# Kernel tuning notes

Hardware: AMD Instinct MI355X
Metric: run time of the kernel (lower is better)

Reference implementation:

```python
import jax, jax.numpy as jnp
import numpy as np

D_MODEL = 2048
N_HEADS = 8
EXPAND_K = 1
EXPAND_V = 2
DK = D_MODEL * EXPAND_K // N_HEADS      # 256 per-head key dim
DV = D_MODEL * EXPAND_V // N_HEADS      # 512 per-head value dim
INTER = 5632
EPS = 1e-6
CHUNK = 64


def setup_inputs() -> dict:
    key = jax.random.key(0)
    ks = jax.random.split(key, 12)
    d = D_MODEL
    s = lambda fan_in: 1.0 / np.sqrt(fan_in)
    return {
        "hidden_states": jax.random.normal(ks[0], (2, 2048, d), jnp.float32),
        "attn_norm_w": jnp.ones((d,), jnp.float32),
        "q_w": jax.random.normal(ks[1], (d, d * EXPAND_K), jnp.float32) * s(d),
        "k_w": jax.random.normal(ks[2], (d, d * EXPAND_K), jnp.float32) * s(d),
        "v_w": jax.random.normal(ks[3], (d, d * EXPAND_V), jnp.float32) * s(d),
        "g_w": jax.random.normal(ks[4], (d, d * EXPAND_V), jnp.float32) * s(d),
        "o_w": jax.random.normal(ks[5], (d * EXPAND_V, d), jnp.float32) * s(d * EXPAND_V),
        "gnorm_w": jnp.ones((DV,), jnp.float32),
        "mlp_norm_w": jnp.ones((d,), jnp.float32),
        "gate_w": jax.random.normal(ks[6], (d, INTER * 2), jnp.float32) * s(d),
        "down_w": jax.random.normal(ks[7], (INTER, d), jnp.float32) * s(INTER),
    }


def rmsnorm(x, w, eps=EPS):
    return x * jax.lax.rsqrt(jnp.mean(x * x, axis=-1, keepdims=True) + eps) * w


def rope(x):
    # x: [B, T, H, D]; non-interleaved rotary on full head dim
    T, D = x.shape[1], x.shape[-1]
    inv_freq = 1.0 / (10000.0 ** (jnp.arange(0, D, 2, dtype=jnp.float32) / D))
    ang = jnp.arange(T, dtype=jnp.float32)[:, None] * inv_freq  # [T, D/2]
    cos = jnp.cos(ang)[None, :, None, :]
    sin = jnp.sin(ang)[None, :, None, :]
    x1, x2 = jnp.split(x, 2, axis=-1)
    return jnp.concatenate([x1 * cos - x2 * sin, x2 * cos + x1 * sin], axis=-1)


def chunk_retention(q, k, v):
    # q,k: [B,T,H,Dk], v: [B,T,H,Dv]; chunkwise-recurrent RetNet retention
    B, T, H, Dk = q.shape
    Dv = v.shape[-1]
    C = CHUNK
    N = T // C
    gamma = 1.0 - jnp.exp2(-5.0 - jnp.arange(H, dtype=jnp.float32))  # [H]
    i = jnp.arange(C, dtype=jnp.float32)
    diff = i[:, None] - i[None, :]
    Dmask = jnp.where(diff >= 0, gamma[:, None, None] ** diff, 0.0)   # [H,C,C]
    cross_decay = gamma[:, None] ** (i[None, :] + 1.0)                # [H,C]
    k_decay = gamma[:, None] ** (C - 1.0 - i[None, :])                # [H,C]
    chunk_decay = gamma ** C                                          # [H]

    # -> [N, B, H, C, D]
    to_chunks = lambda x: jnp.moveaxis(
        x.reshape(B, N, C, H, x.shape[-1]).transpose(0, 1, 3, 2, 4), 1, 0)
    qc, kc, vc = to_chunks(q), to_chunks(k), to_chunks(v)

    def body(S, inp):
        qb, kb, vb = inp  # [B,H,C,Dk/Dv]
        attn = jnp.einsum('bhid,bhjd->bhij', qb, kb) * Dmask
        o_intra = jnp.einsum('bhij,bhje->bhie', attn, vb)
        o_cross = jnp.einsum('bhid,bhde->bhie', qb * cross_decay[None, :, :, None], S)
        S = chunk_decay[None, :, None, None] * S + \
            jnp.einsum('bhid,bhie->bhde', kb * k_decay[None, :, :, None], vb)
        return S, o_intra + o_cross

    S0 = jnp.zeros((B, H, Dk, Dv), q.dtype)
    _, o = jax.lax.scan(body, S0, (qc, kc, vc))  # o: [N,B,H,C,Dv]
    return jnp.moveaxis(o, 0, 1).transpose(0, 1, 3, 2, 4).reshape(B, T, H, Dv)


def reference(hidden_states, attn_norm_w, q_w, k_w, v_w, g_w, o_w, gnorm_w,
              mlp_norm_w, gate_w, down_w):
    B, T, d = hidden_states.shape
    residual = hidden_states
    h = rmsnorm(hidden_states, attn_norm_w)

    # MultiScaleRetention
    q = (h @ q_w).reshape(B, T, N_HEADS, DK)
    k = (h @ k_w).reshape(B, T, N_HEADS, DK)
    v = (h @ v_w).reshape(B, T, N_HEADS, DV)
    g = (h @ g_w).reshape(B, T, N_HEADS, DV)
    q, k = rope(q), rope(k)
    q = q * (DK ** -0.5)
    o = chunk_retention(q, k, v)
    # fused RMSNorm + swish gate (per head over Dv)
    o = rmsnorm(o, gnorm_w) * (g * jax.nn.sigmoid(g))
    h = o.reshape(B, T, N_HEADS * DV) @ o_w

    # fused-residual RMSNorm
    residual = h + residual
    h = rmsnorm(residual, mlp_norm_w)

    # SwiGLU MLP
    y = h @ gate_w
    gate, y = jnp.split(y, 2, axis=-1)
    h = (gate * jax.nn.sigmoid(gate) * y) @ down_w
    return residual + h
```

## Files before the change

kernel.cpp:

```cpp
#include <hip/hip_runtime.h>
#include <cstdint>
#include <cstddef>

typedef unsigned short u16;
typedef __attribute__((ext_vector_type(4))) float f32x4;
typedef __attribute__((ext_vector_type(4))) unsigned int u32x4;

__device__ __forceinline__ float b2f(u16 u) {
  union { unsigned int i; float f; } x; x.i = ((unsigned int)u) << 16; return x.f;
}
__device__ __forceinline__ u16 f2b(float f) {
  union { float f; unsigned int i; } x; x.f = f;
  unsigned int i = x.i;
  i += 0x7fffu + ((i >> 16) & 1u);
  return (u16)(i >> 16);
}

__device__ __forceinline__ void mfma_bf16(f32x4& c, u32x4 a, u32x4 b) {
  asm("v_mfma_f32_16x16x32_bf16 %0, %1, %2, %0" : "+v"(c) : "v"(a), "v"(b));
}

__device__ __forceinline__ void async_ld16(const u16* g, u16* l) {
  typedef __attribute__((address_space(1))) const unsigned int GU;
  typedef __attribute__((address_space(3))) unsigned int LU;
  __builtin_amdgcn_global_load_lds((GU*)g, (LU*)l, 16, 0, 0);
}

__global__ __launch_bounds__(256)
void transpose_cast_kernel(const float* __restrict__ in, u16* __restrict__ out,
                           int K, int N, int ldin) {
  __shared__ float tile[64][65];
  const int nb = N >> 6;
  const int bk = blockIdx.x / nb, bn = blockIdx.x % nb;
  const int k0 = bk * 64, n0 = bn * 64;
  const int tid = threadIdx.x;
#pragma unroll
  for (int p = 0; p < 16; ++p) {
    int idx = p * 256 + tid;
    int r = idx >> 6, c = idx & 63;
    tile[r][c] = in[(size_t)(k0 + r) * ldin + n0 + c];
  }
  __syncthreads();
#pragma unroll
  for (int p = 0; p < 16; ++p) {
    int idx = p * 256 + tid;
    int r = idx >> 6, c = idx & 63;
    out[(size_t)(n0 + r) * K + k0 + c] = f2b(tile[c][r]);
  }
}

__global__ __launch_bounds__(256)
void transpose_k_kernel(const u16* __restrict__ kb, u16* __restrict__ kt) {
  __shared__ u16 tile[64][72];
  const int bid = blockIdx.x;
  const int dd = bid & 3, tt = (bid >> 2) & 31;
  const int h = (bid >> 7) & 7, b = bid >> 10;
  const int t0 = tt * 64, d0 = dd * 64;
  const int tid = threadIdx.x;
#pragma unroll
  for (int p = 0; p < 2; ++p) {
    int idx = p * 256 + tid;
    int r = idx >> 3, cq = (idx & 7) * 8;
    *(uint4*)&tile[r][cq] =
        *(const uint4*)&kb[(size_t)(b * 2048 + t0 + r) * 2048 + h * 256 + d0 + cq];
  }
  __syncthreads();
#pragma unroll
  for (int p = 0; p < 2; ++p) {
    int idx = p * 256 + tid;
    int r = idx >> 3, cq = (idx & 7) * 8;
    union { u16 h8[8]; uint4 v4; } o;
#pragma unroll
    for (int j = 0; j < 8; ++j) o.h8[j] = tile[cq + j][r];
    *(uint4*)&kt[((size_t)(b * 8 + h) * 256 + d0 + r) * 2048 + t0 + cq] = o.v4;
  }
}

__global__ __launch_bounds__(256)
void rmsnorm_cast_kernel(const float* __restrict__ x, const float* __restrict__ w,
                         u16* __restrict__ out) {
  const int row = blockIdx.x, tid = threadIdx.x;
  const float* xr = x + (size_t)row * 2048;
  float4 a = ((const float4*)xr)[tid * 2];
  float4 b = ((const float4*)xr)[tid * 2 + 1];
  float ss = a.x*a.x + a.y*a.y + a.z*a.z + a.w*a.w
           + b.x*b.x + b.y*b.y + b.z*b.z + b.w*b.w;
#pragma unroll
  for (int m = 32; m; m >>= 1) ss += __shfl_xor(ss, m);
  __shared__ float ps[4];
  if ((tid & 63) == 0) ps[tid >> 6] = ss;
  __syncthreads();
  const float sc = rsqrtf((ps[0] + ps[1] + ps[2] + ps[3]) * (1.0f / 2048.0f) + 1e-6f);
  const int base = tid * 8;
  const float vals[8] = {a.x, a.y, a.z, a.w, b.x, b.y, b.z, b.w};
  union { u16 h[8]; uint4 v4[2]; } o;
#pragma unroll
  for (int j = 0; j < 8; ++j) o.h[j] = f2b(vals[j] * sc * w[base + j]);
  *(uint4*)&out[(size_t)row * 2048 + base] = o.v4[0];
  *(uint4*)&out[(size_t)row * 2048 + base + 8] = o.v4[1];
}

__global__ __launch_bounds__(256)
void rmsnorm_bf16_kernel(const u16* __restrict__ x, const float* __restrict__ w,
                         u16* __restrict__ out) {
  const int row = blockIdx.x, tid = threadIdx.x;
  union { uint4 v4; u16 h[8]; } p;
  p.v4 = *(const uint4*)&x[(size_t)row * 2048 + tid * 8];
  float v[8];
  float ss = 0.f;
#pragma unroll
  for (int j = 0; j < 8; ++j) { v[j] = b2f(p.h[j]); ss += v[j] * v[j]; }
#pragma unroll
  for (int m = 32; m; m >>= 1) ss += __shfl_xor(ss, m);
  __shared__ float ps[4];
  if ((tid & 63) == 0) ps[tid >> 6] = ss;
  __syncthreads();
  const float sc = rsqrtf((ps[0] + ps[1] + ps[2] + ps[3]) * (1.0f / 2048.0f) + 1e-6f);
  union { u16 h[8]; uint4 v4; } o;
#pragma unroll
  for (int j = 0; j < 8; ++j) o.h[j] = f2b(v[j] * sc * w[tid * 8 + j]);
  *(uint4*)&out[(size_t)row * 2048 + tid * 8] = o.v4;
}

__global__ __launch_bounds__(256)
void rope_table_kernel(float* __restrict__ ct, float* __restrict__ st) {
  const int idx = blockIdx.x * 256 + threadIdx.x;
  const int t = idx >> 7, i = idx & 127;
  const float e = -(float)i * (0.0078125f * log2f(10000.0f));
  const float ang = (float)t * exp2f(e);
  ct[idx] = cosf(ang);
  st[idx] = sinf(ang);
}

__global__ __launch_bounds__(256)
void rope_apply_kernel(u16* __restrict__ x, const float* __restrict__ ct,
                       const float* __restrict__ st, float scale) {
  const int gid = blockIdx.x * 256 + threadIdx.x;
  const int r = gid >> 8;
  const int rem = gid & 255;
  const int h = rem >> 5;
  const int i4 = (rem & 31) * 4;
  const int t = r & 2047;
  const size_t o1 = (size_t)r * 2048 + h * 256 + i4;
  union { ushort4 v; u16 h4[4]; } p1, p2, q1, q2;
  p1.v = *(ushort4*)&x[o1];
  p2.v = *(ushort4*)&x[o1 + 128];
  const float4 c = *(const float4*)&ct[t * 128 + i4];
  const float4 s = *(const float4*)&st[t * 128 + i4];
  const float cc[4] = {c.x, c.y, c.z, c.w};
  const float sn[4] = {s.x, s.y, s.z, s.w};
#pragma unroll
  for (int j = 0; j < 4; ++j) {
    float x1 = b2f(p1.h4[j]), x2 = b2f(p2.h4[j]);
    q1.h4[j] = f2b((x1 * cc[j] - x2 * sn[j]) * scale);
    q2.h4[j] = f2b((x2 * cc[j] + x1 * sn[j]) * scale);
  }
  *(ushort4*)&x[o1] = q1.v;
  *(ushort4*)&x[o1 + 128] = q2.v;
}

template <int EPI>
__global__ __launch_bounds__(256, 2)
void gemm_bt(const u16* __restrict__ A, const u16* __restrict__ Bt,
             void* Cout, const float* fsrc, const u16* hsrc, int N, int K) {
  __shared__ __align__(16) u16 As[128 * 32];
  __shared__ __align__(16) u16 Bs[128 * 32];
  const int tid = threadIdx.x;
  const int l = tid & 63, w = tid >> 6;
  const int lr = l & 15, hi = l >> 4;
  const int nbn = N >> 7;
  const int bm = blockIdx.x / nbn, bn = blockIdx.x % nbn;
  const int f0 = w * 512 + l * 8;
  const int r0 = f0 >> 5, c0 = f0 & 31;
  const u16* ga0 = A + (size_t)(bm * 128 + r0) * K + c0;
  const u16* ga1 = ga0 + (size_t)64 * K;
  const u16* gb0 = Bt + (size_t)(bn * 128 + r0) * K + c0;
  const u16* gb1 = gb0 + (size_t)64 * K;
  u16* la = As + w * 512;
  u16* lb = Bs + w * 512;
  f32x4 acc[4][4];
#pragma unroll
  for (int m = 0; m < 4; ++m)
#pragma unroll
    for (int n = 0; n < 4; ++n) acc[m][n] = (f32x4){0.f, 0.f, 0.f, 0.f};
  const int wr = (w >> 1) * 64, wc = (w & 1) * 64;
  for (int k0 = 0; k0 < K; k0 += 32) {
    async_ld16(ga0 + k0, la);
    async_ld16(ga1 + k0, la + 2048);
    async_ld16(gb0 + k0, lb);
    async_ld16(gb1 + k0, lb + 2048);
    __syncthreads();
    u32x4 af[4], bfr[4];
#pragma unroll
    for (int m = 0; m < 4; ++m)
      af[m] = *(const u32x4*)&As[(wr + m * 16 + lr) * 32 + hi * 8];
#pragma unroll
    for (int n = 0; n < 4; ++n)
      bfr[n] = *(const u32x4*)&Bs[(wc + n * 16 + lr) * 32 + hi * 8];
#pragma unroll
    for (int m = 0; m < 4; ++m)
#pragma unroll
      for (int n = 0; n < 4; ++n) mfma_bf16(acc[m][n], af[m], bfr[n]);
    __syncthreads();
  }
  const size_t crow0 = (size_t)(bm * 128 + wr);
  const int ccol0 = bn * 128 + wc;
#pragma unroll
  for (int m = 0; m < 4; ++m)
#pragma unroll
    for (int n = 0; n < 4; ++n)
#pragma unroll
      for (int j = 0; j < 4; ++j) {
        size_t r = crow0 + m * 16 + hi * 4 + j;
        size_t c = (size_t)(ccol0 + n * 16 + lr);
        size_t idx = r * N + c;
        float a = acc[m][n][j];
        if (EPI == 1) {
          ((u16*)Cout)[idx] = f2b(a);
        } else if (EPI == 2) {
          ((float*)Cout)[idx] = a + b2f(hsrc[idx]);
        } else if (EPI == 3) {
          float u = b2f(hsrc[idx]);
          ((u16*)Cout)[idx] = f2b(a / (1.0f + expf(-a)) * u);
        } else {
          ((u16*)Cout)[idx] = f2b(a + fsrc[idx]);
        }
      }
}

#define LGK 264
#define LGC 72
__global__ __launch_bounds__(512)
void retention_kernel(const u16* __restrict__ q, const u16* __restrict__ k,
                      const u16* __restrict__ kt, const u16* __restrict__ v,
                      u16* __restrict__ o) {
  __shared__ __align__(16) u16 ks[64 * LGK];
  __shared__ __align__(16) u16 stb[32 * LGK];
  __shared__ __align__(16) u16 ktd[256 * LGC];
  __shared__ __align__(16) u16 vts[32 * LGC];
  __shared__ __align__(16) u16 ab[64 * LGC];
  __shared__ float kdt[64];

  const int tid = threadIdx.x;
  const int l = tid & 63, w = tid >> 6;
  const int lr = l & 15, hi = l >> 4;
  const int wr = w >> 1;
  const int eb = w & 1;
  const int bid = blockIdx.x;
  const int sl = bid & 15;
  const int hh = (bid >> 4) & 7;
  const int b = bid >> 7;
  const float gamma = 1.0f - exp2f(-5.0f - (float)hh);
  const float lg = log2f(gamma);
  const float cdk = exp2f(64.0f * lg);
  const int e0 = sl * 32;

  if (tid < 64) kdt[tid] = exp2f((float)(63 - tid) * lg);
  __syncthreads();

  f32x4 st[4];
#pragma unroll
  for (int t = 0; t < 4; ++t) st[t] = (f32x4){0.f, 0.f, 0.f, 0.f};

  for (int n = 0; n < 32; ++n) {
    const int row0 = b * 2048 + n * 64;
    const int t0 = n * 64;
#pragma unroll
    for (int t = 0; t < 4; ++t)
#pragma unroll
      for (int j = 0; j < 4; ++j)
        stb[(eb * 16 + hi * 4 + j) * LGK + (wr * 4 + t) * 16 + lr] = f2b(st[t][j]);
    u32x4 qf[8];
#pragma unroll
    for (int kk = 0; kk < 8; ++kk)
      qf[kk] = *(const u32x4*)&q[(size_t)(row0 + wr * 16 + lr) * 2048 +
                                 hh * 256 + kk * 32 + hi * 8];
#pragma unroll
    for (int p = 0; p < 4; ++p) {
      int idx = p * 512 + tid;
      int c = idx >> 5, s = (idx & 31) * 8;
      *(uint4*)&ks[c * LGK + s] =
          *(const uint4*)&k[(size_t)(row0 + c) * 2048 + hh * 256 + s];
    }
#pragma unroll
    for (int p = 0; p < 4; ++p) {
      int idx = p * 512 + tid;
      int d = idx >> 3, cq = (idx & 7) * 8;
      union { uint4 v4; u16 h[8]; } pk;
      pk.v4 = *(const uint4*)&kt[((size_t)(b * 8 + hh) * 256 + d) * 2048 + t0 + cq];
      union { u16 h[8]; uint4 v4; } wo;
#pragma unroll
      for (int j2 = 0; j2 < 8; ++j2)
        wo.h[j2] = f2b(b2f(pk.h[j2]) * kdt[cq + j2]);
      *(uint4*)&ktd[d * LGC + cq] = wo.v4;
    }
#pragma unroll
    for (int p = 0; p < 4; ++p) {
      int c = (tid >> 5) + p * 16, e = tid & 31;
      vts[e * LGC + c] = v[(size_t)(row0 + c) * 4096 + hh * 512 + e0 + e];
    }
    __syncthreads();

    f32x4 att[2];
    att[0] = (f32x4){0.f, 0.f, 0.f, 0.f};
    att[1] = (f32x4){0.f, 0.f, 0.f, 0.f};
#pragma unroll
    for (int kk = 0; kk < 8; ++kk) {
#pragma unroll
      for (int jf = 0; jf < 2; ++jf) {
        u32x4 bb = *(const u32x4*)&ks[(eb * 32 + jf * 16 + lr) * LGK + kk * 32 + hi * 8];
        mfma_bf16(att[jf], qf[kk], bb);
      }
    }
#pragma unroll
    for (int jf = 0; jf < 2; ++jf)
#pragma unroll
      for (int j = 0; j < 4; ++j) {
        int i = wr * 16 + hi * 4 + j;
        int jc = eb * 32 + jf * 16 + lr;
        float mv = (i >= jc) ? exp2f((float)(i - jc) * lg) : 0.0f;
        ab[i * LGC + jc] = f2b(att[jf][j] * mv);
      }
    f32x4 occ = (f32x4){0.f, 0.f, 0.f, 0.f};
#pragma unroll
    for (int kk = 0; kk < 8; ++kk) {
      u32x4 bb = *(const u32x4*)&stb[(eb * 16 + lr) * LGK + kk * 32 + hi * 8];
      mfma_bf16(occ, qf[kk], bb);
    }
    __syncthreads();

#pragma unroll
    for (int j = 0; j < 4; ++j) {
      int i = wr * 16 + hi * 4 + j;
      occ[j] *= exp2f((float)(i + 1) * lg);
    }
#pragma unroll
    for (int kk = 0; kk < 2; ++kk) {
      u32x4 aa = *(const u32x4*)&ab[(wr * 16 + lr) * LGC + kk * 32 + hi * 8];
      u32x4 bb = *(const u32x4*)&vts[(eb * 16 + lr) * LGC + kk * 32 + hi * 8];
      mfma_bf16(occ, aa, bb);
    }
#pragma unroll
    for (int j = 0; j < 4; ++j) {
      int i = wr * 16 + hi * 4 + j;
      o[(size_t)(row0 + i) * 4096 + hh * 512 + e0 + eb * 16 + lr] = f2b(occ[j]);
    }
#pragma unroll
    for (int t = 0; t < 4; ++t) {
      st[t][0] *= cdk; st[t][1] *= cdk; st[t][2] *= cdk; st[t][3] *= cdk;
    }
#pragma unroll
    for (int kk = 0; kk < 2; ++kk) {
      u32x4 aa = *(const u32x4*)&vts[(eb * 16 + lr) * LGC + kk * 32 + hi * 8];
#pragma unroll
      for (int t = 0; t < 4; ++t) {
        u32x4 bb = *(const u32x4*)&ktd[((wr * 4 + t) * 16 + lr) * LGC + kk * 32 + hi * 8];
        mfma_bf16(st[t], aa, bb);
      }
    }
    __syncthreads();
  }
}

__global__ __launch_bounds__(64)
void gating_kernel(u16* __restrict__ o, const u16* __restrict__ g,
                   const float* __restrict__ gnw) {
  const int blk = blockIdx.x;
  const size_t base = (size_t)blk * 512;
  const int l = threadIdx.x;
  union { uint4 v4; u16 h[8]; } ov, gv;
  ov.v4 = *(const uint4*)&o[base + l * 8];
  float x[8];
  float ss = 0.f;
#pragma unroll
  for (int j = 0; j < 8; ++j) { x[j] = b2f(ov.h[j]); ss += x[j] * x[j]; }
#pragma unroll
  for (int m = 32; m; m >>= 1) ss += __shfl_xor(ss, m);
  const float sc = rsqrtf(ss * (1.0f / 512.0f) + 1e-6f);
  gv.v4 = *(const uint4*)&g[base + l * 8];
  union { u16 h[8]; uint4 v4; } ou;
#pragma unroll
  for (int j = 0; j < 8; ++j) {
    float gvf = b2f(gv.h[j]);
    float sig = 1.0f / (1.0f + expf(-gvf));
    ou.h[j] = f2b(x[j] * sc * gnw[l * 8 + j] * gvf * sig);
  }
  *(uint4*)&o[base + l * 8] = ou.v4;
}

extern "C" void kernel_launch(void* const* d_in, const int* in_sizes, int n_in,
                              void* d_out, int out_size, void* d_ws, size_t ws_size,
                              hipStream_t stream) {
  (void)in_sizes; (void)n_in; (void)out_size; (void)ws_size;
  const float* hidden      = (const float*)d_in[0];
  const float* attn_norm_w = (const float*)d_in[1];
  const float* q_w         = (const float*)d_in[2];
  const float* k_w         = (const float*)d_in[3];
  const float* v_w         = (const float*)d_in[4];
  const float* g_w         = (const float*)d_in[5];
  const float* o_w         = (const float*)d_in[6];
  const float* gnorm_w     = (const float*)d_in[7];
  const float* mlp_norm_w  = (const float*)d_in[8];
  const float* gate_w      = (const float*)d_in[9];
  const float* down_w      = (const float*)d_in[10];
  float* outp = (float*)d_out;

  char* ws = (char*)d_ws;
  size_t off = 0;
  auto alloc = [&](size_t bytes) -> char* {
    char* p = ws + off;
    off += (bytes + 255) & ~(size_t)255;
    return p;
  };
  u16*   W    = (u16*)alloc(23068672ULL);
  float* ctab = (float*)alloc(1048576ULL);
  float* stab = (float*)alloc(1048576ULL);
  u16*   hb   = (u16*)alloc(16777216ULL);
  u16*   qb   = (u16*)alloc(16777216ULL);
  u16*   kb   = (u16*)alloc(16777216ULL);
  u16*   vb   = (u16*)alloc(33554432ULL);
  u16*   gb   = (u16*)alloc(33554432ULL);
  u16*   ob   = (u16*)alloc(33554432ULL);
  u16*   resb = (u16*)alloc(16777216ULL);
  u16*   ybU  = vb;
  u16*   kt   = W;

  rope_table_kernel<<<1024, 256, 0, stream>>>(ctab, stab);
  rmsnorm_cast_kernel<<<4096, 256, 0, stream>>>(hidden, attn_norm_w, hb);

  transpose_cast_kernel<<<1024, 256, 0, stream>>>(q_w, W, 2048, 2048, 2048);
  gemm_bt<1><<<512, 256, 0, stream>>>(hb, W, (void*)qb, nullptr, nullptr, 2048, 2048);
  transpose_cast_kernel<<<1024, 256, 0, stream>>>(k_w, W, 2048, 2048, 2048);
  gemm_bt<1><<<512, 256, 0, stream>>>(hb, W, (void*)kb, nullptr, nullptr, 2048, 2048);
  transpose_cast_kernel<<<2048, 256, 0, stream>>>(v_w, W, 2048, 4096, 4096);
  gemm_bt<1><<<1024, 256, 0, stream>>>(hb, W, (void*)vb, nullptr, nullptr, 4096, 2048);
  transpose_cast_kernel<<<2048, 256, 0, stream>>>(g_w, W, 2048, 4096, 4096);
  gemm_bt<1><<<1024, 256, 0, stream>>>(hb, W, (void*)gb, nullptr, nullptr, 4096, 2048);

  rope_apply_kernel<<<4096, 256, 0, stream>>>(qb, ctab, stab, 0.0625f);
  rope_apply_kernel<<<4096, 256, 0, stream>>>(kb, ctab, stab, 1.0f);
  transpose_k_kernel<<<2048, 256, 0, stream>>>(kb, kt);

  retention_kernel<<<256, 512, 0, stream>>>(qb, kb, kt, vb, ob);

  gating_kernel<<<32768, 64, 0, stream>>>(ob, gb, gnorm_w);

  transpose_cast_kernel<<<2048, 256, 0, stream>>>(o_w, W, 4096, 2048, 2048);
  gemm_bt<4><<<512, 256, 0, stream>>>(ob, W, (void*)resb, hidden, nullptr, 2048, 4096);

  rmsnorm_bf16_kernel<<<4096, 256, 0, stream>>>(resb, mlp_norm_w, hb);

  transpose_cast_kernel<<<2816, 256, 0, stream>>>(gate_w + 5632, W, 2048, 5632, 11264);
  gemm_bt<1><<<1408, 256, 0, stream>>>(hb, W, (void*)ybU, nullptr, nullptr, 5632, 2048);
  transpose_cast_kernel<<<2816, 256, 0, stream>>>(gate_w, W, 2048, 5632, 11264);
  gemm_bt<3><<<1408, 256, 0, stream>>>(hb, W, (void*)ybU, nullptr, ybU, 5632, 2048);

  transpose_cast_kernel<<<2816, 256, 0, stream>>>(down_w, W, 5632, 2048, 2048);
  gemm_bt<2><<<512, 256, 0, stream>>>(ybU, W, (void*)outp, nullptr, resb, 2048, 5632);
}
```

Before: 1.040 ms.

## Replace GEMM with 4-stage pipelined, swizzled, larger-tile kernel and remap retention blocks

Replaces the single-buffered 128x128 GEMM with a 512-thread kernel that uses BMx256 tiles, a 4-slot LDS ring with async prefetch three k-steps ahead, XOR-swizzled LDS chunks to avoid bank conflicts, MFMA priority raising, and an XCD-aware block index remap. The aim is to hide global load latency behind MFMA work and cut per-iteration barrier stalls. The retention kernel's block-to-(batch, head, slice) mapping is also changed so that neighbouring blocks work on different heads and batches. The cost is a larger LDS footprint, fewer blocks, and a reliance on careful vmcnt/barrier bookkeeping, including a wraparound prefetch that loads redundant tiles at the end of the loop.

```diff
diff --git a/kernel.cpp b/kernel.cpp
--- a/kernel.cpp
+++ b/kernel.cpp
@@ -159,54 +159,108 @@
   *(ushort4*)&x[o1 + 128] = q2.v;
 }
 
-template <int EPI>
-__global__ __launch_bounds__(256, 2)
-void gemm_bt(const u16* __restrict__ A, const u16* __restrict__ Bt,
-             void* Cout, const float* fsrc, const u16* hsrc, int N, int K) {
-  __shared__ __align__(16) u16 As[128 * 32];
-  __shared__ __align__(16) u16 Bs[128 * 32];
+template <int BM, int EPI>
+__global__ __launch_bounds__(512, 2)
+void gemm2(const u16* __restrict__ A, const u16* __restrict__ Bt,
+           void* Cout, const float* fsrc, const u16* hsrc, int N, int K) {
+  constexpr int MF = BM / 32;
+  constexpr int WROWS = BM / 2;
+  constexpr int LA = BM / 128;
+  constexpr int SLOTA = BM * 32;
+  constexpr int SLOTB = 256 * 32;
+  constexpr int SLOT = SLOTA + SLOTB;
+  constexpr int VM2 = 2 * (LA + 2);
+  __shared__ __align__(16) u16 lds[4 * SLOT];
+
   const int tid = threadIdx.x;
   const int l = tid & 63, w = tid >> 6;
   const int lr = l & 15, hi = l >> 4;
-  const int nbn = N >> 7;
-  const int bm = blockIdx.x / nbn, bn = blockIdx.x % nbn;
-  const int f0 = w * 512 + l * 8;
-  const int r0 = f0 >> 5, c0 = f0 & 31;
-  const u16* ga0 = A + (size_t)(bm * 128 + r0) * K + c0;
-  const u16* ga1 = ga0 + (size_t)64 * K;
-  const u16* gb0 = Bt + (size_t)(bn * 128 + r0) * K + c0;
-  const u16* gb1 = gb0 + (size_t)64 * K;
-  u16* la = As + w * 512;
-  u16* lb = Bs + w * 512;
-  f32x4 acc[4][4];
-#pragma unroll
-  for (int m = 0; m < 4; ++m)
+  const int wm = w >> 2, wn = w & 3;
+  const int nbn = N >> 8;
+  int bid;
+  { int cpx = (int)gridDim.x >> 3; int ob = blockIdx.x;
+    bid = (ob & 7) * cpx + (ob >> 3); }
+  const int bm = bid / nbn, bn = bid % nbn;
+  const int nt = K >> 5;
+
+  size_t asrc[LA]; int adst[LA];
+#pragma unroll
+  for (int t = 0; t < LA; ++t) {
+    int gi = t * 512 + tid;
+    int row = gi >> 2;
+    int ch = (gi & 3) ^ (row & 3);
+    asrc[t] = (size_t)(bm * BM + row) * K + ch * 8;
+    adst[t] = (t * 512 + w * 64) * 8;
+  }
+  size_t bsrc[2]; int bdst[2];
+#pragma unroll
+  for (int t = 0; t < 2; ++t) {
+    int gi = t * 512 + tid;
+    int row = gi >> 2;
+    int ch = (gi & 3) ^ (row & 3);
+    bsrc[t] = (size_t)(bn * 256 + row) * K + ch * 8;
+    bdst[t] = SLOTA + (t * 512 + w * 64) * 8;
+  }
+  const int xch = (hi ^ (lr & 3)) << 3;
+  int aoff[MF], boff[4];
+#pragma unroll
+  for (int m = 0; m < MF; ++m)
+    aoff[m] = (wm * WROWS + m * 16 + lr) * 32 + xch;
+#pragma unroll
+  for (int n = 0; n < 4; ++n)
+    boff[n] = SLOTA + (wn * 64 + n * 16 + lr) * 32 + xch;
+
+  f32x4 acc[MF][4];
+#pragma unroll
+  for (int m = 0; m < MF; ++m)
 #pragma unroll
     for (int n = 0; n < 4; ++n) acc[m][n] = (f32x4){0.f, 0.f, 0.f, 0.f};
-  const int wr = (w >> 1) * 64, wc = (w & 1) * 64;
-  for (int k0 = 0; k0 < K; k0 += 32) {
-    async_ld16(ga0 + k0, la);
-    async_ld16(ga1 + k0, la + 2048);
-    async_ld16(gb0 + k0, lb);
-    async_ld16(gb1 + k0, lb + 2048);
-    __syncthreads();
-    u32x4 af[4], bfr[4];
-#pragma unroll
-    for (int m = 0; m < 4; ++m)
-      af[m] = *(const u32x4*)&As[(wr + m * 16 + lr) * 32 + hi * 8];
-#pragma unroll
-    for (int n = 0; n < 4; ++n)
-      bfr[n] = *(const u32x4*)&Bs[(wc + n * 16 + lr) * 32 + hi * 8];
-#pragma unroll
-    for (int m = 0; m < 4; ++m)
-#pragma unroll
-      for (int n = 0; n < 4; ++n) mfma_bf16(acc[m][n], af[m], bfr[n]);
-    __syncthreads();
-  }
-  const size_t crow0 = (size_t)(bm * 128 + wr);
-  const int ccol0 = bn * 128 + wc;
-#pragma unroll
-  for (int m = 0; m < 4; ++m)
+
+  auto stage = [&](int kt, int s) {
+    const int sb = s * SLOT;
+#pragma unroll
+    for (int t = 0; t < LA; ++t)
+      async_ld16(A + (asrc[t] + kt * 32), &lds[sb + adst[t]]);
+#pragma unroll
+    for (int t = 0; t < 2; ++t)
+      async_ld16(Bt + (bsrc[t] + kt * 32), &lds[sb + bdst[t]]);
+  };
+
+  stage(0, 0); __builtin_amdgcn_sched_barrier(0);
+  stage(1, 1); __builtin_amdgcn_sched_barrier(0);
+  stage(2, 2); __builtin_amdgcn_sched_barrier(0);
+  asm volatile("s_waitcnt vmcnt(%0)" :: "n"(VM2) : "memory");
+  __builtin_amdgcn_sched_barrier(0);
+  __builtin_amdgcn_s_barrier();
+  __builtin_amdgcn_sched_barrier(0);
+
+  for (int i = 0; i < nt; ++i) {
+    int pf = i + 3; if (pf >= nt) pf -= nt;
+    stage(pf, (i + 3) & 3);
+    __builtin_amdgcn_sched_barrier(0);
+    const int sb = (i & 3) * SLOT;
+    u32x4 af[MF], bf[4];
+#pragma unroll
+    for (int m = 0; m < MF; ++m) af[m] = *(const u32x4*)&lds[sb + aoff[m]];
+#pragma unroll
+    for (int n = 0; n < 4; ++n) bf[n] = *(const u32x4*)&lds[sb + boff[n]];
+    __builtin_amdgcn_s_setprio(1);
+#pragma unroll
+    for (int m = 0; m < MF; ++m)
+#pragma unroll
+      for (int n = 0; n < 4; ++n) mfma_bf16(acc[m][n], af[m], bf[n]);
+    __builtin_amdgcn_s_setprio(0);
+    __builtin_amdgcn_sched_barrier(0);
+    asm volatile("s_waitcnt vmcnt(%0)" :: "n"(VM2) : "memory");
+    __builtin_amdgcn_sched_barrier(0);
+    __builtin_amdgcn_s_barrier();
+    __builtin_amdgcn_sched_barrier(0);
+  }
+
+  const size_t crow0 = (size_t)(bm * BM + wm * WROWS);
+  const int ccol0 = bn * 256 + wn * 64;
+#pragma unroll
+  for (int m = 0; m < MF; ++m)
 #pragma unroll
     for (int n = 0; n < 4; ++n)
 #pragma unroll
@@ -247,9 +301,10 @@
   const int wr = w >> 1;
   const int eb = w & 1;
   const int bid = blockIdx.x;
-  const int sl = bid & 15;
-  const int hh = (bid >> 4) & 7;
-  const int b = bid >> 7;
+  const int g = bid & 15;
+  const int sl = bid >> 4;
+  const int hh = g & 7;
+  const int b = g >> 3;
   const float gamma = 1.0f - exp2f(-5.0f - (float)hh);
   const float lg = log2f(gamma);
   const float cdk = exp2f(64.0f * lg);
@@ -429,13 +484,13 @@
   rmsnorm_cast_kernel<<<4096, 256, 0, stream>>>(hidden, attn_norm_w, hb);
 
   transpose_cast_kernel<<<1024, 256, 0, stream>>>(q_w, W, 2048, 2048, 2048);
-  gemm_bt<1><<<512, 256, 0, stream>>>(hb, W, (void*)qb, nullptr, nullptr, 2048, 2048);
+  gemm2<128, 1><<<256, 512, 0, stream>>>(hb, W, (void*)qb, nullptr, nullptr, 2048, 2048);
   transpose_cast_kernel<<<1024, 256, 0, stream>>>(k_w, W, 2048, 2048, 2048);
-  gemm_bt<1><<<512, 256, 0, stream>>>(hb, W, (void*)kb, nullptr, nullptr, 2048, 2048);
+  gemm2<128, 1><<<256, 512, 0, stream>>>(hb, W, (void*)kb, nullptr, nullptr, 2048, 2048);
   transpose_cast_kernel<<<2048, 256, 0, stream>>>(v_w, W, 2048, 4096, 4096);
-  gemm_bt<1><<<1024, 256, 0, stream>>>(hb, W, (void*)vb, nullptr, nullptr, 4096, 2048);
+  gemm2<256, 1><<<256, 512, 0, stream>>>(hb, W, (void*)vb, nullptr, nullptr, 4096, 2048);
   transpose_cast_kernel<<<2048, 256, 0, stream>>>(g_w, W, 2048, 4096, 4096);
-  gemm_bt<1><<<1024, 256, 0, stream>>>(hb, W, (void*)gb, nullptr, nullptr, 4096, 2048);
+  gemm2<256, 1><<<256, 512, 0, stream>>>(hb, W, (void*)gb, nullptr, nullptr, 4096, 2048);
 
   rope_apply_kernel<<<4096, 256, 0, stream>>>(qb, ctab, stab, 0.0625f);
   rope_apply_kernel<<<4096, 256, 0, stream>>>(kb, ctab, stab, 1.0f);
@@ -446,15 +501,15 @@
   gating_kernel<<<32768, 64, 0, stream>>>(ob, gb, gnorm_w);
 
   transpose_cast_kernel<<<2048, 256, 0, stream>>>(o_w, W, 4096, 2048, 2048);
-  gemm_bt<4><<<512, 256, 0, stream>>>(ob, W, (void*)resb, hidden, nullptr, 2048, 4096);
+  gemm2<128, 4><<<256, 512, 0, stream>>>(ob, W, (void*)resb, hidden, nullptr, 2048, 4096);
 
   rmsnorm_bf16_kernel<<<4096, 256, 0, stream>>>(resb, mlp_norm_w, hb);
 
   transpose_cast_kernel<<<2816, 256, 0, stream>>>(gate_w + 5632, W, 2048, 5632, 11264);
-  gemm_bt<1><<<1408, 256, 0, stream>>>(hb, W, (void*)ybU, nullptr, nullptr, 5632, 2048);
+  gemm2<128, 1><<<704, 512, 0, stream>>>(hb, W, (void*)ybU, nullptr, nullptr, 5632, 2048);
   transpose_cast_kernel<<<2816, 256, 0, stream>>>(gate_w, W, 2048, 5632, 11264);
-  gemm_bt<3><<<1408, 256, 0, stream>>>(hb, W, (void*)ybU, nullptr, ybU, 5632, 2048);
+  gemm2<128, 3><<<704, 512, 0, stream>>>(hb, W, (void*)ybU, nullptr, ybU, 5632, 2048);
 
   transpose_cast_kernel<<<2816, 256, 0, stream>>>(down_w, W, 5632, 2048, 2048);
-  gemm_bt<2><<<512, 256, 0, stream>>>(ybU, W, (void*)outp, nullptr, resb, 2048, 5632);
-}
+  gemm2<128, 2><<<256, 512, 0, stream>>>(ybU, W, (void*)outp, nullptr, resb, 2048, 5632);
+}
```

New measurement: 961.0 us. 7.6% less time.
